# Optimization experiments

Measured on AMD Instinct MI355X. Metric: run time of the kernel, lower is better.

Reference implementation:

```python
import jax, jax.numpy as jnp
import numpy as np

SR = 48000
N_FFT = 2048
HOP = 960
N_MELS = 64
FMIN, FMAX = 20.0, 16000.0
N_DIR = 2304
B = 8
N_SAMPLES = 960000
EPS = 1e-8


def _hz_to_mel(hz):
    return 2595.0 * np.log10(1.0 + hz / 700.0)


def _mel_to_hz(mel):
    return 700.0 * (10.0 ** (mel / 2595.0) - 1.0)


def _build_mel_filterbank(n_fft, n_mels, sr, fmin, fmax):
    n_freqs = n_fft // 2 + 1
    fft_freqs = np.linspace(0.0, sr / 2.0, n_freqs)
    mel_points = np.linspace(_hz_to_mel(fmin), _hz_to_mel(fmax), n_mels + 2)
    hz_points = np.array([_mel_to_hz(m) for m in mel_points])
    fb = np.zeros((n_mels, n_freqs), dtype=np.float32)
    for m in range(1, n_mels + 1):
        f_low, f_ctr, f_high = hz_points[m - 1], hz_points[m], hz_points[m + 1]
        lower = (fft_freqs - f_low) / max(f_ctr - f_low, 1e-8)
        upper = (f_high - fft_freqs) / max(f_high - f_ctr, 1e-8)
        fb[m - 1, :] = np.maximum(0.0, np.minimum(lower, upper))
    return fb


def setup_inputs() -> dict:
    key = jax.random.key(0)
    k1, k2, k3, k4, k5, k6 = jax.random.split(key, 6)
    F_ = N_FFT // 2 + 1
    waveform = jax.random.normal(k1, (B, 2, N_SAMPLES), dtype=jnp.float32)
    W_real = jax.random.normal(k2, (N_DIR, F_), dtype=jnp.float32)
    W_imag = jax.random.normal(k3, (N_DIR, F_), dtype=jnp.float32)
    norm_hr_sq = jax.random.uniform(k4, (N_DIR, F_), dtype=jnp.float32)
    norm_hl_sq = jax.random.uniform(k5, (N_DIR, F_), dtype=jnp.float32)
    az_bin_idx = jax.random.randint(k6, (N_DIR,), 0, N_MELS)
    # deterministic buffers as in the torch module
    n = jnp.arange(N_FFT, dtype=jnp.float32)
    window = 0.5 - 0.5 * jnp.cos(2.0 * jnp.pi * n / N_FFT)  # torch.hann_window (periodic)
    mel_fb = jnp.asarray(_build_mel_filterbank(N_FFT, N_MELS, SR, FMIN, FMAX))
    return {"waveform": waveform, "W_real": W_real, "W_imag": W_imag,
            "norm_hr_sq": norm_hr_sq, "norm_hl_sq": norm_hl_sq,
            "az_bin_idx": az_bin_idx, "window": window, "mel_fb": mel_fb}


def _stft(x, window):
    # x: [B, N] -> complex [B, F, T]
    pad = N_FFT // 2
    xp = jnp.pad(x, ((0, 0), (pad, pad)))
    T = 1 + (xp.shape[-1] - N_FFT) // HOP
    starts = jnp.arange(T) * HOP
    frames = xp[:, starts[:, None] + jnp.arange(N_FFT)]  # [B, T, n_fft]
    spec = jnp.fft.rfft(frames * window, axis=-1)        # [B, T, F]
    return jnp.transpose(spec, (0, 2, 1))                # [B, F, T]


def reference(waveform, W_real, W_imag, norm_hr_sq, norm_hl_sq, az_bin_idx, window, mel_fb):
    x_L = waveform[:, 0, :]
    x_R = waveform[:, 1, :]
    X_L = _stft(x_L, window)  # [B, F, T] complex
    X_R = _stft(x_R, window)
    pow_L = jnp.abs(X_L) ** 2
    pow_R = jnp.abs(X_R) ** 2

    mel_L = jnp.einsum('mf,bft->bmt', mel_fb, pow_L)
    mel_R = jnp.einsum('mf,bft->bmt', mel_fb, pow_R)
    ch0 = 10.0 * jnp.log10(mel_L + EPS)
    ch1 = 10.0 * jnp.log10(mel_R + EPS)
    ch2 = 10.0 * jnp.log10(mel_L / (mel_R + EPS) + EPS)

    csd = X_L * jnp.conj(X_R)
    csd_r, csd_i = jnp.real(csd), jnp.imag(csd)
    mel_csd_r = jnp.einsum('mf,bft->bmt', mel_fb, csd_r)
    mel_csd_i = jnp.einsum('mf,bft->bmt', mel_fb, csd_i)
    mel_csd_norm = jnp.sqrt(mel_csd_r ** 2 + mel_csd_i ** 2 + EPS)
    ch3 = mel_csd_i / mel_csd_norm
    ch4 = mel_csd_r / mel_csd_norm

    # per-direction HRTF cross-correlation, then scatter into azimuth bins
    corr_un = (jnp.einsum('df,bft->bdt', W_real, csd_r)
               - jnp.einsum('df,bft->bdt', W_imag, csd_i))  # [B, N_DIR, T]
    n1 = jnp.einsum('df,bft->bdt', norm_hr_sq, pow_L)
    n2 = jnp.einsum('df,bft->bdt', norm_hl_sq, pow_R)
    corr = corr_un / jnp.sqrt(n1 * n2 + 1e-8)

    T = corr.shape[-1]
    hrtf = jnp.zeros((corr.shape[0], N_MELS, T), dtype=corr.dtype)
    hrtf = hrtf.at[:, az_bin_idx, :].add(corr)
    cnt = jnp.zeros((N_MELS,), dtype=corr.dtype).at[az_bin_idx].add(1.0)
    ch5 = hrtf / (cnt[None, :, None] + EPS)

    return jnp.stack([ch0, ch1, ch2, ch3, ch4, ch5], axis=1)  # [B, 6, 64, T]
```

## Files before the change

### kernel.cpp

```cpp
#include <hip/hip_runtime.h>
#include <math.h>

#define NFFT    2048
#define HOP     960
#define NMELS   64
#define NDIR    2304
#define BATCH   8
#define NSAMP   960000
#define NF      1025
#define TFRAMES 1001
#define TP      1024
#define SEG     1056
#define K2      2112
#define BKM     16
#define LDT     68
#define NWG     1152

typedef unsigned short ushort_t;
typedef __attribute__((ext_vector_type(8))) short bf16x8;
typedef __attribute__((ext_vector_type(4))) float f32x4;

__device__ __forceinline__ ushort_t f2b(float x) {
  unsigned u = __float_as_uint(x);
  return (ushort_t)((u + 0x7FFFu + ((u >> 16) & 1u)) >> 16);
}
__device__ __forceinline__ float b2f(unsigned h) {
  return __uint_as_float(h << 16);
}

#define N_HRTF ((size_t)BATCH * NMELS * TFRAMES)
#define N_MF   ((size_t)NMELS * SEG)
#define N_CORR ((size_t)BATCH * NDIR * TP)
#define N_FC   ((size_t)BATCH * TP * K2)
#define N_P    ((size_t)BATCH * TP * SEG)
#define N_AC   ((size_t)NDIR * K2)
#define N_AH   ((size_t)NDIR * SEG)

__global__ __launch_bounds__(256) void prep_k(
    const float* __restrict__ Wr, const float* __restrict__ Wi,
    const float* __restrict__ Hr, const float* __restrict__ Hl,
    const float* __restrict__ mfb,
    ushort_t* __restrict__ ACh, ushort_t* __restrict__ AHrh,
    ushort_t* __restrict__ AHlh, float* __restrict__ MFp)
{
  const size_t n1 = (size_t)NDIR * K2, n2 = (size_t)NDIR * SEG;
  const size_t tot = n1 + 2 * n2 + (size_t)NMELS * SEG;
  for (size_t idx = blockIdx.x * 256 + threadIdx.x; idx < tot; idx += (size_t)gridDim.x * 256) {
    if (idx < n1) {
      int d = idx / K2, k2 = idx - (size_t)d * K2;
      float w;
      if (k2 < SEG) w = (k2 < NF) ? Wr[(size_t)d * NF + k2] : 0.0f;
      else { int kk = k2 - SEG; w = (kk < NF) ? -Wi[(size_t)d * NF + kk] : 0.0f; }
      ACh[idx] = f2b(w);
    } else if (idx < n1 + n2) {
      size_t i = idx - n1; int d = i / SEG, k = i - (size_t)d * SEG;
      AHrh[i] = f2b((k < NF) ? Hr[(size_t)d * NF + k] : 0.0f);
    } else if (idx < n1 + 2 * n2) {
      size_t i = idx - n1 - n2; int d = i / SEG, k = i - (size_t)d * SEG;
      AHlh[i] = f2b((k < NF) ? Hl[(size_t)d * NF + k] : 0.0f);
    } else {
      size_t i = idx - n1 - 2 * n2; int m = i / SEG, k = i - (size_t)m * SEG;
      MFp[i] = (k < NF) ? mfb[(size_t)m * NF + k] : 0.0f;
    }
  }
}

__global__ __launch_bounds__(256) void stft_kernel(
    const float* __restrict__ wave, const float* __restrict__ window,
    ushort_t* __restrict__ PLh, ushort_t* __restrict__ PRh,
    ushort_t* __restrict__ FCh, ushort_t* __restrict__ FCl)
{
  __shared__ float b0r[NFFT], b0i[NFFT], b1r[NFFT], b1i[NFFT];
  __shared__ float twr[NFFT / 2], twi[NFFT / 2];

  const int tid = threadIdx.x;
  const int bt  = blockIdx.x;
  const int b   = bt / TFRAMES;
  const int t   = bt - b * TFRAMES;

  for (int j = tid; j < NFFT / 2; j += 256) {
    float ang = -6.283185307179586f * (float)j / (float)NFFT;
    float sv, cv; sincosf(ang, &sv, &cv);
    twr[j] = cv; twi[j] = sv;
  }
  const float* wL = wave + ((size_t)b * 2 + 0) * NSAMP;
  const float* wR = wave + ((size_t)b * 2 + 1) * NSAMP;
  for (int j = tid; j < NFFT; j += 256) {
    int s0 = t * HOP - (NFFT / 2) + j;
    float wv = window[j];
    float vr = 0.0f, vi = 0.0f;
    if (s0 >= 0 && s0 < NSAMP) { vr = wL[s0] * wv; vi = wR[s0] * wv; }
    b0r[j] = vr; b0i[j] = vi;
  }
  __syncthreads();

  float *sr = b0r, *si = b0i, *dr = b1r, *di = b1i;
  int s = 1;
  for (int stage = 0; stage < 11; ++stage) {
    #pragma unroll 4
    for (int i = tid; i < NFFT / 2; i += 256) {
      int ps = i & ~(s - 1), q = i & (s - 1);
      float wr = twr[ps], wi = twi[ps];
      float ar = sr[i], ai = si[i];
      float br = sr[i + NFFT / 2], bi = si[i + NFFT / 2];
      int d0 = (ps << 1) + q;
      dr[d0] = ar + br; di[d0] = ai + bi;
      float xr = ar - br, xi = ai - bi;
      dr[d0 + s] = xr * wr - xi * wi;
      di[d0 + s] = xr * wi + xi * wr;
    }
    __syncthreads();
    float* tp = sr; sr = dr; dr = tp;
    tp = si; si = di; di = tp;
    s <<= 1;
  }

  const size_t rb = (size_t)b * TP + t;
  for (int f = tid; f < SEG; f += 256) {
    float pl = 0.f, pr = 0.f, cr = 0.f, ci = 0.f;
    if (f < NF) {
      int fc = (NFFT - f) & (NFFT - 1);
      float ar = sr[f], ai = si[f];
      float br = sr[fc], bi = si[fc];
      float lr = 0.5f * (ar + br), li = 0.5f * (ai - bi);
      float rr = 0.5f * (ai + bi), ri = 0.5f * (br - ar);
      pl = lr * lr + li * li;
      pr = rr * rr + ri * ri;
      cr = lr * rr + li * ri;
      ci = li * rr - lr * ri;
    }
    PLh[rb * SEG + f] = f2b(pl);
    PRh[rb * SEG + f] = f2b(pr);
    ushort_t crh = f2b(cr), cih = f2b(ci);
    FCh[rb * K2 + f]       = crh;
    FCh[rb * K2 + SEG + f] = cih;
    FCl[rb * K2 + f]       = f2b(cr - b2f(crh));
    FCl[rb * K2 + SEG + f] = f2b(ci - b2f(cih));
  }
}

#define GL16(gp, loff) \
  __builtin_amdgcn_global_load_lds((const __attribute__((address_space(1))) void*)(gp), \
      (__attribute__((address_space(3))) void*)(smem + (loff)), 16, 0, 0)

#define XCD_DECODE() \
  int logical = (blockIdx.x & 7) * (NWG / 8) + (blockIdx.x >> 3); \
  int dt = logical % 18; int rq = logical / 18;                   \
  int tt = rq & 7; int b = rq >> 3;                               \
  const int d0 = dt * 128; const int t0 = tt * 128;

__global__ __launch_bounds__(256, 3) void gemm_c(
    const ushort_t* __restrict__ A, const ushort_t* __restrict__ B,
    ushort_t* __restrict__ Cout)
{
  __shared__ __align__(16) char smem[16384];
  const int tid = threadIdx.x;
  const int wave = tid >> 6, lane = tid & 63;
  XCD_DECODE();
  const int wr = wave >> 1, wc = wave & 1;

  const int srow = lane >> 2, skb = (lane & 3) * 8;
  const int c0 = wave, c1 = wave + 4;
  const size_t ar0 = (size_t)(d0 + c0 * 16 + srow) * K2 + skb;
  const size_t ar1 = (size_t)(d0 + c1 * 16 + srow) * K2 + skb;
  const size_t br0 = ((size_t)b * TP + t0 + c0 * 16 + srow) * K2 + skb;
  const size_t br1 = ((size_t)b * TP + t0 + c1 * 16 + srow) * K2 + skb;

  f32x4 acc[4][4];
  #pragma unroll
  for (int i = 0; i < 4; ++i)
    #pragma unroll
    for (int j = 0; j < 4; ++j) acc[i][j] = (f32x4){0.f, 0.f, 0.f, 0.f};

  const int frow = (lane & 15) * 64, fk = (lane >> 4) * 16;

  for (int k0 = 0; k0 < K2; k0 += 32) {
    GL16(A + ar0 + k0, 0    + c0 * 1024);
    GL16(A + ar1 + k0, 0    + c1 * 1024);
    GL16(B + br0 + k0, 8192 + c0 * 1024);
    GL16(B + br1 + k0, 8192 + c1 * 1024);
    __syncthreads();
    bf16x8 af[4], bf[4];
    #pragma unroll
    for (int f = 0; f < 4; ++f) {
      af[f] = *(const bf16x8*)(smem +        wr * 4096 + f * 1024 + frow + fk);
      bf[f] = *(const bf16x8*)(smem + 8192 + wc * 4096 + f * 1024 + frow + fk);
    }
    #pragma unroll
    for (int i = 0; i < 4; ++i)
      #pragma unroll
      for (int j = 0; j < 4; ++j)
        acc[i][j] = __builtin_amdgcn_mfma_f32_16x16x32_bf16(af[i], bf[j], acc[i][j], 0, 0, 0);
    __syncthreads();
  }

  const int orow = (lane >> 4) * 4, ocol = lane & 15;
  #pragma unroll
  for (int i = 0; i < 4; ++i) {
    int d = d0 + wr * 64 + i * 16 + orow;
    #pragma unroll
    for (int j = 0; j < 4; ++j) {
      int t = t0 + wc * 64 + j * 16 + ocol;
      ushort_t* p = Cout + ((size_t)b * NDIR + d) * TP + t;
      #pragma unroll
      for (int r = 0; r < 4; ++r) p[(size_t)r * TP] = f2b(acc[i][j][r]);
    }
  }
}

__global__ __launch_bounds__(256, 3) void gemm_n1(
    const ushort_t* __restrict__ A, const ushort_t* __restrict__ B,
    ushort_t* __restrict__ N1)
{
  __shared__ __align__(16) char smem[16384];
  const int tid = threadIdx.x;
  const int wave = tid >> 6, lane = tid & 63;
  XCD_DECODE();
  const int wr = wave >> 1, wc = wave & 1;

  const int srow = lane >> 2, skb = (lane & 3) * 8;
  const int c0 = wave, c1 = wave + 4;
  const size_t ar0 = (size_t)(d0 + c0 * 16 + srow) * SEG + skb;
  const size_t ar1 = (size_t)(d0 + c1 * 16 + srow) * SEG + skb;
  const size_t br0 = ((size_t)b * TP + t0 + c0 * 16 + srow) * SEG + skb;
  const size_t br1 = ((size_t)b * TP + t0 + c1 * 16 + srow) * SEG + skb;

  f32x4 acc[4][4];
  #pragma unroll
  for (int i = 0; i < 4; ++i)
    #pragma unroll
    for (int j = 0; j < 4; ++j) acc[i][j] = (f32x4){0.f, 0.f, 0.f, 0.f};

  const int frow = (lane & 15) * 64, fk = (lane >> 4) * 16;

  for (int k0 = 0; k0 < SEG; k0 += 32) {
    GL16(A + ar0 + k0, 0    + c0 * 1024);
    GL16(A + ar1 + k0, 0    + c1 * 1024);
    GL16(B + br0 + k0, 8192 + c0 * 1024);
    GL16(B + br1 + k0, 8192 + c1 * 1024);
    __syncthreads();
    bf16x8 af[4], bf[4];
    #pragma unroll
    for (int f = 0; f < 4; ++f) {
      af[f] = *(const bf16x8*)(smem +        wr * 4096 + f * 1024 + frow + fk);
      bf[f] = *(const bf16x8*)(smem + 8192 + wc * 4096 + f * 1024 + frow + fk);
    }
    #pragma unroll
    for (int i = 0; i < 4; ++i)
      #pragma unroll
      for (int j = 0; j < 4; ++j)
        acc[i][j] = __builtin_amdgcn_mfma_f32_16x16x32_bf16(af[i], bf[j], acc[i][j], 0, 0, 0);
    __syncthreads();
  }

  const int orow = (lane >> 4) * 4, ocol = lane & 15;
  #pragma unroll
  for (int i = 0; i < 4; ++i) {
    int d = d0 + wr * 64 + i * 16 + orow;
    #pragma unroll
    for (int j = 0; j < 4; ++j) {
      int t = t0 + wc * 64 + j * 16 + ocol;
      ushort_t* p = N1 + ((size_t)b * NDIR + d) * TP + t;
      #pragma unroll
      for (int r = 0; r < 4; ++r) p[(size_t)r * TP] = f2b(acc[i][j][r]);
    }
  }
}

__global__ __launch_bounds__(256, 3) void gemm_n2(
    const ushort_t* __restrict__ A, const ushort_t* __restrict__ B,
    const ushort_t* __restrict__ CU, const ushort_t* __restrict__ N1,
    const int* __restrict__ az, float* __restrict__ hrtf)
{
  __shared__ __align__(16) char smem[16384];
  const int tid = threadIdx.x;
  const int wave = tid >> 6, lane = tid & 63;
  XCD_DECODE();
  const int wr = wave >> 1, wc = wave & 1;

  const int srow = lane >> 2, skb = (lane & 3) * 8;
  const int c0 = wave, c1 = wave + 4;
  const size_t ar0 = (size_t)(d0 + c0 * 16 + srow) * SEG + skb;
  const size_t ar1 = (size_t)(d0 + c1 * 16 + srow) * SEG + skb;
  const size_t br0 = ((size_t)b * TP + t0 + c0 * 16 + srow) * SEG + skb;
  const size_t br1 = ((size_t)b * TP + t0 + c1 * 16 + srow) * SEG + skb;

  f32x4 acc[4][4];
  #pragma unroll
  for (int i = 0; i < 4; ++i)
    #pragma unroll
    for (int j = 0; j < 4; ++j) acc[i][j] = (f32x4){0.f, 0.f, 0.f, 0.f};

  const int frow = (lane & 15) * 64, fk = (lane >> 4) * 16;

  for (int k0 = 0; k0 < SEG; k0 += 32) {
    GL16(A + ar0 + k0, 0    + c0 * 1024);
    GL16(A + ar1 + k0, 0    + c1 * 1024);
    GL16(B + br0 + k0, 8192 + c0 * 1024);
    GL16(B + br1 + k0, 8192 + c1 * 1024);
    __syncthreads();
    bf16x8 af[4], bf[4];
    #pragma unroll
    for (int f = 0; f < 4; ++f) {
      af[f] = *(const bf16x8*)(smem +        wr * 4096 + f * 1024 + frow + fk);
      bf[f] = *(const bf16x8*)(smem + 8192 + wc * 4096 + f * 1024 + frow + fk);
    }
    #pragma unroll
    for (int i = 0; i < 4; ++i)
      #pragma unroll
      for (int j = 0; j < 4; ++j)
        acc[i][j] = __builtin_amdgcn_mfma_f32_16x16x32_bf16(af[i], bf[j], acc[i][j], 0, 0, 0);
    __syncthreads();
  }

  const int orow = (lane >> 4) * 4, ocol = lane & 15;
  #pragma unroll
  for (int i = 0; i < 4; ++i) {
    int dbase = d0 + wr * 64 + i * 16 + orow;
    #pragma unroll
    for (int j = 0; j < 4; ++j) {
      int t = t0 + wc * 64 + j * 16 + ocol;
      if (t < TFRAMES) {
        #pragma unroll
        for (int r = 0; r < 4; ++r) {
          int d = dbase + r;
          size_t off = ((size_t)b * NDIR + d) * TP + t;
          float n1v = b2f(N1[off]);
          float n2v = acc[i][j][r];
          float cu  = b2f(CU[off]);
          float cval = cu / sqrtf(n1v * n2v + 1e-8f);
          unsafeAtomicAdd(hrtf + ((size_t)b * NMELS + az[d]) * TFRAMES + t, cval);
        }
      }
    }
  }
}

__global__ __launch_bounds__(256) void mel_gemm(
    const float* __restrict__ MF,
    const ushort_t* __restrict__ PLh, const ushort_t* __restrict__ PRh,
    const ushort_t* __restrict__ FCh, const ushort_t* __restrict__ FCl,
    float* __restrict__ out)
{
  __shared__ float As[BKM][LDT];
  __shared__ float Bs[4][BKM][LDT];
  const int b  = blockIdx.y;
  const int t0 = blockIdx.x * 64;
  const int tid = threadIdx.x;
  const int tx = tid & 15, ty = tid >> 4;
  const int lr = tid >> 2, lk = (tid & 3) * 4;

  float aL[4][4] = {}, aR[4][4] = {}, aC[4][4] = {}, aI[4][4] = {};

  const size_t rb = (size_t)b * TP + t0 + lr;
  const ushort_t* Bp[4] = {PLh, PRh, FCh, FCh + SEG};
  const ushort_t* Bl[4] = {PLh, PRh, FCl, FCl + SEG};
  const size_t   Bst[4] = {SEG, SEG, K2, K2};

  for (int k0 = 0; k0 < SEG; k0 += BKM) {
    {
      float4 a = *(const float4*)(MF + (size_t)lr * SEG + k0 + lk);
      As[lk + 0][lr] = a.x; As[lk + 1][lr] = a.y;
      As[lk + 2][lr] = a.z; As[lk + 3][lr] = a.w;
    }
    #pragma unroll
    for (int m = 0; m < 4; ++m) {
      uint2 v = *(const uint2*)(Bp[m] + rb * Bst[m] + k0 + lk);
      float f0 = b2f(v.x & 0xffffu), f1 = b2f(v.x >> 16);
      float f2 = b2f(v.y & 0xffffu), f3 = b2f(v.y >> 16);
      if (m >= 2) {
        uint2 w = *(const uint2*)(Bl[m] + rb * Bst[m] + k0 + lk);
        f0 += b2f(w.x & 0xffffu); f1 += b2f(w.x >> 16);
        f2 += b2f(w.y & 0xffffu); f3 += b2f(w.y >> 16);
      }
      Bs[m][lk + 0][lr] = f0; Bs[m][lk + 1][lr] = f1;
      Bs[m][lk + 2][lr] = f2; Bs[m][lk + 3][lr] = f3;
    }
    __syncthreads();
    #pragma unroll
    for (int kk = 0; kk < BKM; ++kk) {
      float4 mf4 = *(const float4*)&As[kk][ty << 2];
      float4 pl4 = *(const float4*)&Bs[0][kk][tx << 2];
      float4 pr4 = *(const float4*)&Bs[1][kk][tx << 2];
      float4 cr4 = *(const float4*)&Bs[2][kk][tx << 2];
      float4 ci4 = *(const float4*)&Bs[3][kk][tx << 2];
      const float* mf = (const float*)&mf4;
      const float* pl = (const float*)&pl4; const float* pr = (const float*)&pr4;
      const float* cr = (const float*)&cr4; const float* ci = (const float*)&ci4;
      #pragma unroll
      for (int i = 0; i < 4; ++i)
        #pragma unroll
        for (int j = 0; j < 4; ++j) {
          aL[i][j] = fmaf(mf[i], pl[j], aL[i][j]);
          aR[i][j] = fmaf(mf[i], pr[j], aR[i][j]);
          aC[i][j] = fmaf(mf[i], cr[j], aC[i][j]);
          aI[i][j] = fmaf(mf[i], ci[j], aI[i][j]);
        }
    }
    __syncthreads();
  }

  #pragma unroll
  for (int i = 0; i < 4; ++i) {
    int m = (ty << 2) + i;
    #pragma unroll
    for (int j = 0; j < 4; ++j) {
      int t = t0 + (tx << 2) + j;
      if (t < TFRAMES) {
        float mlv = aL[i][j], mrv = aR[i][j], crv = aC[i][j], civ = aI[i][j];
        float ch0 = 10.0f * log10f(mlv + 1e-8f);
        float ch1 = 10.0f * log10f(mrv + 1e-8f);
        float ch2 = 10.0f * log10f(mlv / (mrv + 1e-8f) + 1e-8f);
        float nrm = sqrtf(crv * crv + civ * civ + 1e-8f);
        float ch3 = civ / nrm;
        float ch4 = crv / nrm;
        size_t bb = (size_t)b * 6 * NMELS;
        out[(bb + 0 * NMELS + m) * TFRAMES + t] = ch0;
        out[(bb + 1 * NMELS + m) * TFRAMES + t] = ch1;
        out[(bb + 2 * NMELS + m) * TFRAMES + t] = ch2;
        out[(bb + 3 * NMELS + m) * TFRAMES + t] = ch3;
        out[(bb + 4 * NMELS + m) * TFRAMES + t] = ch4;
      }
    }
  }
}

__global__ __launch_bounds__(256) void finalize_k(
    const float* __restrict__ hrtf, const int* __restrict__ az,
    float* __restrict__ out)
{
  __shared__ int red[256];
  const int m = blockIdx.x, b = blockIdx.y, tid = threadIdx.x;
  int c = 0;
  for (int j = tid; j < NDIR; j += 256) c += (az[j] == m) ? 1 : 0;
  red[tid] = c;
  __syncthreads();
  for (int st = 128; st > 0; st >>= 1) {
    if (tid < st) red[tid] += red[tid + st];
    __syncthreads();
  }
  float inv = 1.0f / ((float)red[0] + 1e-8f);
  const float* src = hrtf + ((size_t)b * NMELS + m) * TFRAMES;
  float* dst = out + (((size_t)b * 6 + 5) * NMELS + m) * TFRAMES;
  for (int t = tid; t < TFRAMES; t += 256) dst[t] = src[t] * inv;
}

extern "C" void kernel_launch(void* const* d_in, const int* in_sizes, int n_in,
                              void* d_out, int out_size, void* d_ws, size_t ws_size,
                              hipStream_t stream) {
  const float* wave   = (const float*)d_in[0];
  const float* W_real = (const float*)d_in[1];
  const float* W_imag = (const float*)d_in[2];
  const float* Nhr    = (const float*)d_in[3];
  const float* Nhl    = (const float*)d_in[4];
  const int*   az     = (const int*)  d_in[5];
  const float* window = (const float*)d_in[6];
  const float* mel_fb = (const float*)d_in[7];
  float* out = (float*)d_out;

  float* fw      = (float*)d_ws;
  float* hrtf    = fw;
  float* MFp     = hrtf + N_HRTF;
  ushort_t* ub   = (ushort_t*)(MFp + N_MF);
  ushort_t* corr = ub;
  ushort_t* n1b  = corr + N_CORR;
  ushort_t* FCh  = n1b + N_CORR;
  ushort_t* FCl  = FCh + N_FC;
  ushort_t* PLh  = FCl + N_FC;
  ushort_t* PRh  = PLh + N_P;
  ushort_t* ACh  = PRh + N_P;
  ushort_t* AHrh = ACh + N_AC;
  ushort_t* AHlh = AHrh + N_AH;

  hipMemsetAsync(hrtf, 0, sizeof(float) * N_HRTF, stream);

  prep_k<<<2048, 256, 0, stream>>>(W_real, W_imag, Nhr, Nhl, mel_fb,
                                   ACh, AHrh, AHlh, MFp);

  stft_kernel<<<BATCH * TFRAMES, 256, 0, stream>>>(wave, window, PLh, PRh, FCh, FCl);

  gemm_c <<<NWG, 256, 0, stream>>>(ACh, FCh, corr);
  gemm_n1<<<NWG, 256, 0, stream>>>(AHrh, PLh, n1b);
  gemm_n2<<<NWG, 256, 0, stream>>>(AHlh, PRh, corr, n1b, az, hrtf);

  mel_gemm<<<dim3(16, BATCH), 256, 0, stream>>>(MFp, PLh, PRh, FCh, FCl, out);

  finalize_k<<<dim3(NMELS, BATCH), 256, 0, stream>>>(hrtf, az, out);
}
```

Before: 757.4 us.

## Fuse n1 and n2 GEMMs into one kernel with LDS-staged azimuth scatter

Merges the two normalisation GEMMs into a single kernel that keeps both accumulators in registers, so the bf16 n1 intermediate is no longer written to and re-read from global memory and one launch disappears. The azimuth scatter now first accumulates into a per-workgroup LDS histogram, then issues one global atomic per mel/time cell instead of one per direction. The cost is doubled accumulator registers and larger LDS, with occupancy lowered from 3 to 2 workgroups per CU, which may reduce latency hiding in the main loop.

```diff
diff --git a/kernel.cpp b/kernel.cpp
--- a/kernel.cpp
+++ b/kernel.cpp
@@ -208,11 +208,13 @@
   }
 }
 
-__global__ __launch_bounds__(256, 3) void gemm_n1(
-    const ushort_t* __restrict__ A, const ushort_t* __restrict__ B,
-    ushort_t* __restrict__ N1)
-{
-  __shared__ __align__(16) char smem[16384];
+__global__ __launch_bounds__(256, 2) void gemm_n12(
+    const ushort_t* __restrict__ A1, const ushort_t* __restrict__ A2,
+    const ushort_t* __restrict__ B1, const ushort_t* __restrict__ B2,
+    const ushort_t* __restrict__ CU, const int* __restrict__ az,
+    float* __restrict__ hrtf)
+{
+  __shared__ __align__(16) char smem[34816];
   const int tid = threadIdx.x;
   const int wave = tid >> 6, lane = tid & 63;
   XCD_DECODE();
@@ -225,113 +227,81 @@
   const size_t br0 = ((size_t)b * TP + t0 + c0 * 16 + srow) * SEG + skb;
   const size_t br1 = ((size_t)b * TP + t0 + c1 * 16 + srow) * SEG + skb;
 
-  f32x4 acc[4][4];
+  f32x4 acc1[4][4], acc2[4][4];
   #pragma unroll
   for (int i = 0; i < 4; ++i)
     #pragma unroll
-    for (int j = 0; j < 4; ++j) acc[i][j] = (f32x4){0.f, 0.f, 0.f, 0.f};
+    for (int j = 0; j < 4; ++j) {
+      acc1[i][j] = (f32x4){0.f, 0.f, 0.f, 0.f};
+      acc2[i][j] = (f32x4){0.f, 0.f, 0.f, 0.f};
+    }
 
   const int frow = (lane & 15) * 64, fk = (lane >> 4) * 16;
 
   for (int k0 = 0; k0 < SEG; k0 += 32) {
-    GL16(A + ar0 + k0, 0    + c0 * 1024);
-    GL16(A + ar1 + k0, 0    + c1 * 1024);
-    GL16(B + br0 + k0, 8192 + c0 * 1024);
-    GL16(B + br1 + k0, 8192 + c1 * 1024);
-    __syncthreads();
-    bf16x8 af[4], bf[4];
+    GL16(A1 + ar0 + k0, 0     + c0 * 1024);
+    GL16(A1 + ar1 + k0, 0     + c1 * 1024);
+    GL16(A2 + ar0 + k0, 8192  + c0 * 1024);
+    GL16(A2 + ar1 + k0, 8192  + c1 * 1024);
+    GL16(B1 + br0 + k0, 16384 + c0 * 1024);
+    GL16(B1 + br1 + k0, 16384 + c1 * 1024);
+    GL16(B2 + br0 + k0, 24576 + c0 * 1024);
+    GL16(B2 + br1 + k0, 24576 + c1 * 1024);
+    __syncthreads();
+    bf16x8 a1f[4], a2f[4], b1f[4], b2f[4];
     #pragma unroll
     for (int f = 0; f < 4; ++f) {
-      af[f] = *(const bf16x8*)(smem +        wr * 4096 + f * 1024 + frow + fk);
-      bf[f] = *(const bf16x8*)(smem + 8192 + wc * 4096 + f * 1024 + frow + fk);
+      a1f[f] = *(const bf16x8*)(smem +         wr * 4096 + f * 1024 + frow + fk);
+      a2f[f] = *(const bf16x8*)(smem + 8192  + wr * 4096 + f * 1024 + frow + fk);
+      b1f[f] = *(const bf16x8*)(smem + 16384 + wc * 4096 + f * 1024 + frow + fk);
+      b2f[f] = *(const bf16x8*)(smem + 24576 + wc * 4096 + f * 1024 + frow + fk);
     }
     #pragma unroll
     for (int i = 0; i < 4; ++i)
       #pragma unroll
-      for (int j = 0; j < 4; ++j)
-        acc[i][j] = __builtin_amdgcn_mfma_f32_16x16x32_bf16(af[i], bf[j], acc[i][j], 0, 0, 0);
-    __syncthreads();
-  }
-
-  const int orow = (lane >> 4) * 4, ocol = lane & 15;
-  #pragma unroll
-  for (int i = 0; i < 4; ++i) {
-    int d = d0 + wr * 64 + i * 16 + orow;
-    #pragma unroll
-    for (int j = 0; j < 4; ++j) {
-      int t = t0 + wc * 64 + j * 16 + ocol;
-      ushort_t* p = N1 + ((size_t)b * NDIR + d) * TP + t;
-      #pragma unroll
-      for (int r = 0; r < 4; ++r) p[(size_t)r * TP] = f2b(acc[i][j][r]);
-    }
-  }
-}
-
-__global__ __launch_bounds__(256, 3) void gemm_n2(
-    const ushort_t* __restrict__ A, const ushort_t* __restrict__ B,
-    const ushort_t* __restrict__ CU, const ushort_t* __restrict__ N1,
-    const int* __restrict__ az, float* __restrict__ hrtf)
-{
-  __shared__ __align__(16) char smem[16384];
-  const int tid = threadIdx.x;
-  const int wave = tid >> 6, lane = tid & 63;
-  XCD_DECODE();
-  const int wr = wave >> 1, wc = wave & 1;
-
-  const int srow = lane >> 2, skb = (lane & 3) * 8;
-  const int c0 = wave, c1 = wave + 4;
-  const size_t ar0 = (size_t)(d0 + c0 * 16 + srow) * SEG + skb;
-  const size_t ar1 = (size_t)(d0 + c1 * 16 + srow) * SEG + skb;
-  const size_t br0 = ((size_t)b * TP + t0 + c0 * 16 + srow) * SEG + skb;
-  const size_t br1 = ((size_t)b * TP + t0 + c1 * 16 + srow) * SEG + skb;
-
-  f32x4 acc[4][4];
-  #pragma unroll
-  for (int i = 0; i < 4; ++i)
-    #pragma unroll
-    for (int j = 0; j < 4; ++j) acc[i][j] = (f32x4){0.f, 0.f, 0.f, 0.f};
-
-  const int frow = (lane & 15) * 64, fk = (lane >> 4) * 16;
-
-  for (int k0 = 0; k0 < SEG; k0 += 32) {
-    GL16(A + ar0 + k0, 0    + c0 * 1024);
-    GL16(A + ar1 + k0, 0    + c1 * 1024);
-    GL16(B + br0 + k0, 8192 + c0 * 1024);
-    GL16(B + br1 + k0, 8192 + c1 * 1024);
-    __syncthreads();
-    bf16x8 af[4], bf[4];
-    #pragma unroll
-    for (int f = 0; f < 4; ++f) {
-      af[f] = *(const bf16x8*)(smem +        wr * 4096 + f * 1024 + frow + fk);
-      bf[f] = *(const bf16x8*)(smem + 8192 + wc * 4096 + f * 1024 + frow + fk);
-    }
-    #pragma unroll
-    for (int i = 0; i < 4; ++i)
-      #pragma unroll
-      for (int j = 0; j < 4; ++j)
-        acc[i][j] = __builtin_amdgcn_mfma_f32_16x16x32_bf16(af[i], bf[j], acc[i][j], 0, 0, 0);
-    __syncthreads();
-  }
+      for (int j = 0; j < 4; ++j) {
+        acc1[i][j] = __builtin_amdgcn_mfma_f32_16x16x32_bf16(a1f[i], b1f[j], acc1[i][j], 0, 0, 0);
+        acc2[i][j] = __builtin_amdgcn_mfma_f32_16x16x32_bf16(a2f[i], b2f[j], acc2[i][j], 0, 0, 0);
+      }
+    __syncthreads();
+  }
+
+  __syncthreads();
+  float* lh = (float*)smem;
+  for (int e = tid; e < 64 * 132; e += 256) lh[e] = 0.0f;
+  __syncthreads();
 
   const int orow = (lane >> 4) * 4, ocol = lane & 15;
   #pragma unroll
   for (int i = 0; i < 4; ++i) {
     int dbase = d0 + wr * 64 + i * 16 + orow;
+    int azv[4];
+    #pragma unroll
+    for (int r = 0; r < 4; ++r) azv[r] = az[dbase + r];
     #pragma unroll
     for (int j = 0; j < 4; ++j) {
-      int t = t0 + wc * 64 + j * 16 + ocol;
+      int tl = wc * 64 + j * 16 + ocol;
+      int t  = t0 + tl;
       if (t < TFRAMES) {
         #pragma unroll
         for (int r = 0; r < 4; ++r) {
           int d = dbase + r;
-          size_t off = ((size_t)b * NDIR + d) * TP + t;
-          float n1v = b2f(N1[off]);
-          float n2v = acc[i][j][r];
-          float cu  = b2f(CU[off]);
+          float n1v = acc1[i][j][r], n2v = acc2[i][j][r];
+          float cu  = b2f(CU[((size_t)b * NDIR + d) * TP + t]);
           float cval = cu / sqrtf(n1v * n2v + 1e-8f);
-          unsafeAtomicAdd(hrtf + ((size_t)b * NMELS + az[d]) * TFRAMES + t, cval);
+          atomicAdd(&lh[azv[r] * 132 + tl], cval);
         }
       }
+    }
+  }
+  __syncthreads();
+
+  for (int e = tid; e < NMELS * 128; e += 256) {
+    int m = e >> 7, tc = e & 127;
+    int t = t0 + tc;
+    if (t < TFRAMES) {
+      float v = lh[m * 132 + tc];
+      unsafeAtomicAdd(hrtf + ((size_t)b * NMELS + m) * TFRAMES + t, v);
     }
   }
 }
@@ -463,8 +433,7 @@
   float* MFp     = hrtf + N_HRTF;
   ushort_t* ub   = (ushort_t*)(MFp + N_MF);
   ushort_t* corr = ub;
-  ushort_t* n1b  = corr + N_CORR;
-  ushort_t* FCh  = n1b + N_CORR;
+  ushort_t* FCh  = corr + N_CORR;
   ushort_t* FCl  = FCh + N_FC;
   ushort_t* PLh  = FCl + N_FC;
   ushort_t* PRh  = PLh + N_P;
@@ -479,9 +448,8 @@
 
   stft_kernel<<<BATCH * TFRAMES, 256, 0, stream>>>(wave, window, PLh, PRh, FCh, FCl);
 
-  gemm_c <<<NWG, 256, 0, stream>>>(ACh, FCh, corr);
-  gemm_n1<<<NWG, 256, 0, stream>>>(AHrh, PLh, n1b);
-  gemm_n2<<<NWG, 256, 0, stream>>>(AHlh, PRh, corr, n1b, az, hrtf);
+  gemm_c  <<<NWG, 256, 0, stream>>>(ACh, FCh, corr);
+  gemm_n12<<<NWG, 256, 0, stream>>>(AHrh, AHlh, PLh, PRh, corr, az, hrtf);
 
   mel_gemm<<<dim3(16, BATCH), 256, 0, stream>>>(MFp, PLh, PRh, FCh, FCl, out);
 
```

New measurement: 764.5 us. About the same (+0.9%).

## Stage CU/N1 tiles in LDS and pre-reduce hrtf scatter in shared memory

Applied to the files above, without the earlier changes.

The gemm_n2 epilogue now loads the CU and N1 tiles into LDS with coalesced 16-byte loads in four quarter passes, instead of doing scattered 2-byte global reads per accumulator element. Each block accumulates its azimuth-binned results into a shared 64x128 histogram with LDS atomics, then flushes it once with global atomics. This cuts the number of global atomics from one per direction to one per mel bin per frame. In exchange, LDS use grows to about 49 KB per block, which may reduce occupancy below the launch bound of 3, and the epilogue gains extra syncs.

```diff
diff --git a/kernel.cpp b/kernel.cpp
--- a/kernel.cpp
+++ b/kernel.cpp
@@ -272,7 +272,7 @@
     const ushort_t* __restrict__ CU, const ushort_t* __restrict__ N1,
     const int* __restrict__ az, float* __restrict__ hrtf)
 {
-  __shared__ __align__(16) char smem[16384];
+  __shared__ __align__(16) char smem[50176];
   const int tid = threadIdx.x;
   const int wave = tid >> 6, lane = tid & 63;
   XCD_DECODE();
@@ -313,25 +313,58 @@
     __syncthreads();
   }
 
+  float* lh = (float*)(smem + 16384);
+  const ushort_t* lu = (const ushort_t*)smem;
+  for (int e = tid; e < 64 * 132; e += 256) lh[e] = 0.0f;
+  __syncthreads();
+
   const int orow = (lane >> 4) * 4, ocol = lane & 15;
-  #pragma unroll
-  for (int i = 0; i < 4; ++i) {
-    int dbase = d0 + wr * 64 + i * 16 + orow;
-    #pragma unroll
-    for (int j = 0; j < 4; ++j) {
-      int t = t0 + wc * 64 + j * 16 + ocol;
-      if (t < TFRAMES) {
+
+  for (int q = 0; q < 4; ++q) {
+    #pragma unroll
+    for (int c = 0; c < 2; ++c) {
+      size_t ge = ((size_t)b * NDIR + d0 + q * 32 + c * 16 + wave * 4 + (lane >> 4)) * TP
+                  + t0 + (lane & 15) * 8;
+      GL16(CU + ge, 0    + c * 4096 + wave * 1024);
+      GL16(N1 + ge, 8192 + c * 4096 + wave * 1024);
+    }
+    __syncthreads();
+
+    if (wr == (q >> 1)) {
+      #pragma unroll
+      for (int i2 = 0; i2 < 2; ++i2) {
+        int i = (q & 1) * 2 + i2;
+        int dq0 = i2 * 16 + orow;
+        int azv[4];
         #pragma unroll
-        for (int r = 0; r < 4; ++r) {
-          int d = dbase + r;
-          size_t off = ((size_t)b * NDIR + d) * TP + t;
-          float n1v = b2f(N1[off]);
-          float n2v = acc[i][j][r];
-          float cu  = b2f(CU[off]);
-          float cval = cu / sqrtf(n1v * n2v + 1e-8f);
-          unsafeAtomicAdd(hrtf + ((size_t)b * NMELS + az[d]) * TFRAMES + t, cval);
+        for (int r = 0; r < 4; ++r) azv[r] = az[d0 + q * 32 + dq0 + r];
+        #pragma unroll
+        for (int j = 0; j < 4; ++j) {
+          int tl = wc * 64 + j * 16 + ocol;
+          int t  = t0 + tl;
+          if (t < TFRAMES) {
+            #pragma unroll
+            for (int r = 0; r < 4; ++r) {
+              int dq = dq0 + r;
+              float cu  = b2f(lu[dq * 128 + tl]);
+              float n1v = b2f(lu[4096 + dq * 128 + tl]);
+              float n2v = acc[i][j][r];
+              float cval = cu / sqrtf(n1v * n2v + 1e-8f);
+              atomicAdd(&lh[azv[r] * 132 + tl], cval);
+            }
+          }
         }
       }
+    }
+    __syncthreads();
+  }
+
+  for (int e = tid; e < NMELS * 128; e += 256) {
+    int m = e >> 7, tc = e & 127;
+    int t = t0 + tc;
+    if (t < TFRAMES) {
+      float v = lh[m * 132 + tc];
+      unsafeAtomicAdd(hrtf + ((size_t)b * NMELS + m) * TFRAMES + t, v);
     }
   }
 }
```

Measured after the change: 1.104 ms. 1.46x slower.
